# Kernel tuning notes

Measured on AMD Instinct MI355X. Metric: run time of the kernel, lower is better.

## Reference

```python
import jax, jax.numpy as jnp
import numpy as np

N = 1024          # n_nodes
E = 32768         # n_edges (includes N self-loops)
EMBED = 256       # embed_dim
NHEAD = 8
NHID = EMBED // NHEAD  # 32
SLOPE = 0.2       # leaky_relu negative slope
NEG = -1e30       # mask value (finite to keep grads clean)


def setup_inputs() -> dict:
    key = jax.random.key(0)
    k1, k2, k3, k4, k5 = jax.random.split(key, 5)
    h = jax.random.normal(k1, (N, EMBED), dtype=jnp.float32)
    # self-loops first so every destination row has >=1 unmasked edge
    loops = jnp.stack([jnp.arange(N, dtype=jnp.int32)] * 2, axis=1)
    rnd = jax.random.randint(k2, (E - N, 2), 0, N, dtype=jnp.int32)
    edge_index = jnp.concatenate([loops, rnd], axis=0)  # [E, 2] = (r, c)
    W_l = jax.random.normal(k3, (EMBED, NHEAD * NHID), jnp.float32) / np.sqrt(EMBED).astype(np.float32)
    W_r = jax.random.normal(k4, (EMBED, NHEAD * NHID), jnp.float32) / np.sqrt(EMBED).astype(np.float32)
    attn_w = jax.random.normal(k5, (NHID,), jnp.float32) / np.sqrt(NHID).astype(np.float32)
    return {"h": h, "edge_index": edge_index, "W_l": W_l, "W_r": W_r, "attn_w": attn_w}


def reference(h, edge_index, W_l, W_r, attn_w):
    n = h.shape[0]
    g_l = (h @ W_l).reshape(n, NHEAD, NHID)  # [N, H, D]
    g_r = (h @ W_r).reshape(n, NHEAD, NHID)  # [N, H, D]
    # dense all-pairs GATv2 score: g_sum[i, j] = g_l[j] + g_r[i]
    # (matches g_l.repeat(n,1,1) + g_r.repeat_interleave(n, dim=0))
    g_sum = g_l[None, :, :, :] + g_r[:, None, :, :]            # [N, N, H, D]
    e = jnp.einsum('ijhd,d->ijh', jax.nn.leaky_relu(g_sum, SLOPE), attn_w)  # [N, N, H]
    # edge mask: keep only (r, c) pairs present in edge_index
    adj = jnp.zeros((n, n), dtype=bool).at[edge_index[:, 0], edge_index[:, 1]].set(True)
    e = jnp.where(adj[:, :, None], e, NEG)
    a = jax.nn.softmax(e, axis=1)                               # softmax over source nodes j
    # attention-weighted aggregation of source features, concat heads
    out = jnp.einsum('ijh,jhd->ihd', a, g_l).reshape(n, NHEAD * NHID)  # [N, EMBED]
    return out
```

## Files before the change

kernel.cpp:

```cpp
#include <hip/hip_runtime.h>
#include <hip/hip_bf16.h>
#include <stdint.h>

#define NN 1024
#define EMBED 256
#define NHEAD 8
#define NHID 32
#define SLOPE 0.2f

__global__ __launch_bounds__(256) void k_prep(const float* __restrict__ h,
                                              const float* __restrict__ Wl,
                                              const float* __restrict__ Wr,
                                              const int* __restrict__ ei, int E,
                                              float* __restrict__ gl,
                                              float* __restrict__ gr,
                                              unsigned int* __restrict__ adj) {
    const int blk = blockIdx.x;
    const int t = threadIdx.x;

    if (blk < 128) {
        const int z  = blk & 1;
        const int bn = ((blk >> 1) & 3) * 64;
        const int bm = (blk >> 3) * 64;
        const float* W = z ? Wr : Wl;
        float* out = z ? gr : gl;
        const int tx = t & 15;
        const int ty = t >> 4;

        __shared__ float As[16][65];
        __shared__ float Bs[16][65];

        const int ar = t >> 2, ac = (t & 3) << 2;
        const int br = t >> 4, bc = (t & 15) << 2;
        const float* Aptr = &h[(bm + ar) * EMBED + ac];
        const float* Bptr = &W[br * EMBED + bn + bc];

        float acc[4][4];
#pragma unroll
        for (int i = 0; i < 4; ++i)
#pragma unroll
            for (int j = 0; j < 4; ++j) acc[i][j] = 0.f;

        float4 a_reg = *reinterpret_cast<const float4*>(Aptr);
        float4 b_reg = *reinterpret_cast<const float4*>(Bptr);

        for (int k0 = 0; k0 < EMBED; k0 += 16) {
            As[ac + 0][ar] = a_reg.x; As[ac + 1][ar] = a_reg.y;
            As[ac + 2][ar] = a_reg.z; As[ac + 3][ar] = a_reg.w;
            Bs[br][bc + 0] = b_reg.x; Bs[br][bc + 1] = b_reg.y;
            Bs[br][bc + 2] = b_reg.z; Bs[br][bc + 3] = b_reg.w;
            __syncthreads();
            if (k0 + 16 < EMBED) {
                a_reg = *reinterpret_cast<const float4*>(Aptr + k0 + 16);
                b_reg = *reinterpret_cast<const float4*>(Bptr + (size_t)(k0 + 16) * EMBED);
            }
#pragma unroll
            for (int kk = 0; kk < 16; ++kk) {
                float a[4], b[4];
#pragma unroll
                for (int i = 0; i < 4; ++i) a[i] = As[kk][ty * 4 + i];
#pragma unroll
                for (int j = 0; j < 4; ++j) b[j] = Bs[kk][tx * 4 + j];
#pragma unroll
                for (int i = 0; i < 4; ++i)
#pragma unroll
                    for (int j = 0; j < 4; ++j) acc[i][j] += a[i] * b[j];
            }
            __syncthreads();
        }
#pragma unroll
        for (int i = 0; i < 4; ++i) {
            float4 v = make_float4(acc[i][0], acc[i][1], acc[i][2], acc[i][3]);
            *reinterpret_cast<float4*>(&out[(bm + ty * 4 + i) * EMBED + bn + tx * 4]) = v;
        }
    } else {
        const int lo = (blk - 128) * 8;
        __shared__ unsigned int lads[256];
        lads[t] = 0u;
        __syncthreads();

        const int4* ei4 = reinterpret_cast<const int4*>(ei);
        const int nvec = E >> 1;
        int base = 0;
        for (; base + 1024 <= nvec; base += 1024) {
            int4 v0 = ei4[base + t];
            int4 v1 = ei4[base + t + 256];
            int4 v2 = ei4[base + t + 512];
            int4 v3 = ei4[base + t + 768];
#pragma unroll
            for (int u = 0; u < 4; ++u) {
                int4 v = (u == 0) ? v0 : (u == 1) ? v1 : (u == 2) ? v2 : v3;
                int r0 = v.x - lo;
                if ((unsigned)r0 < 8u)
                    atomicOr(&lads[r0 * 32 + ((unsigned)v.y >> 5)], 1u << (v.y & 31));
                int r1 = v.z - lo;
                if ((unsigned)r1 < 8u)
                    atomicOr(&lads[r1 * 32 + ((unsigned)v.w >> 5)], 1u << (v.w & 31));
            }
        }
        for (int idx = base + t; idx < nvec; idx += 256) {
            int4 v = ei4[idx];
            int r0 = v.x - lo;
            if ((unsigned)r0 < 8u)
                atomicOr(&lads[r0 * 32 + ((unsigned)v.y >> 5)], 1u << (v.y & 31));
            int r1 = v.z - lo;
            if ((unsigned)r1 < 8u)
                atomicOr(&lads[r1 * 32 + ((unsigned)v.w >> 5)], 1u << (v.w & 31));
        }
        __syncthreads();
        adj[lo * 32 + t] = lads[t];
    }
}

__global__ __launch_bounds__(256) void k_attn(const float* __restrict__ gl,
                                              const float* __restrict__ gr,
                                              const unsigned int* __restrict__ adj,
                                              const float* __restrict__ attn_w,
                                              float* __restrict__ out) {
    const int i = blockIdx.x;
    const int t = threadIdx.x;

    __shared__ int nbr[NN];
    __shared__ int cnt_s;

    if (t < 64) {
        unsigned int w = (t < 32) ? adj[i * 32 + t] : 0u;
        int c = __popc(w);
        int pre = c;
#pragma unroll
        for (int d = 1; d < 64; d <<= 1) {
            int v = __shfl_up(pre, d);
            if (t >= d) pre += v;
        }
        int off = pre - c;
        if (t == 63) cnt_s = pre;
        while (w) {
            int b = __builtin_ctz(w);
            w &= w - 1;
            nbr[off++] = t * 32 + b;
        }
    }
    __syncthreads();

    const int cnt = cnt_s;
    const float grv = gr[i * EMBED + t];
    const float aw = attn_w[t & 31];

    float m = -3e38f;
    float s = 0.f;
    float acc = 0.f;

    float g[4];
#pragma unroll
    for (int u = 0; u < 4; ++u) {
        int e = u < cnt ? u : 0;
        g[u] = gl[nbr[e] * EMBED + t];
    }

    for (int e0 = 0; e0 < cnt; e0 += 4) {
        float cg[4];
#pragma unroll
        for (int u = 0; u < 4; ++u) cg[u] = g[u];
#pragma unroll
        for (int u = 0; u < 4; ++u) {
            int e = e0 + 4 + u;
            e = e < cnt ? e : 0;
            g[u] = gl[nbr[e] * EMBED + t];
        }
        float p[4];
#pragma unroll
        for (int u = 0; u < 4; ++u) {
            float x = cg[u] + grv;
            float pv = (x > 0.f ? x : SLOPE * x) * aw;
            pv += __shfl_xor(pv, 1);
            pv += __shfl_xor(pv, 2);
            pv += __shfl_xor(pv, 4);
            pv += __shfl_xor(pv, 8);
            pv += __shfl_xor(pv, 16);
            p[u] = pv;
        }
#pragma unroll
        for (int u = 0; u < 4; ++u) {
            if (e0 + u < cnt) {
                float mn = fmaxf(m, p[u]);
                float sc = __expf(m - mn);
                float ev = __expf(p[u] - mn);
                s = s * sc + ev;
                acc = acc * sc + ev * cg[u];
                m = mn;
            }
        }
    }
    out[i * EMBED + t] = acc / s;
}

extern "C" void kernel_launch(void* const* d_in, const int* in_sizes, int n_in,
                              void* d_out, int out_size, void* d_ws, size_t ws_size,
                              hipStream_t stream) {
    const float* h  = (const float*)d_in[0];
    const int*   ei = (const int*)d_in[1];
    const float* Wl = (const float*)d_in[2];
    const float* Wr = (const float*)d_in[3];
    const float* aw = (const float*)d_in[4];
    float* out = (float*)d_out;
    const int E = in_sizes[1] / 2;

    unsigned int* adj = (unsigned int*)d_ws;
    float* gl = (float*)((char*)d_ws + 131072);
    float* gr = gl + NN * EMBED;

    k_prep<<<256, 256, 0, stream>>>(h, Wl, Wr, ei, E, gl, gr, adj);
    k_attn<<<NN, 256, 0, stream>>>(gl, gr, adj, aw, out);
}
```

Baseline: 36.41 us.

## Rebalance prep kernel: smaller GEMM tiles, fewer wider adjacency-build blocks

The GEMM part now uses 32x64 output tiles, so it runs on 256 blocks instead of 128, with each thread computing a 2x4 micro-tile. Only half the threads load the A tile. The adjacency part drops from 128 blocks of 8 rows to 32 blocks of 32 rows, which cuts the redundant full scans of edge_index by a factor of four. The intent is to spread GEMM work across more CUs and shrink total edge-scan traffic. In exchange, each GEMM thread does less reuse per load, and the new scan loop assumes nvec is a multiple of 2048, with the remainder loop removed.

Measured after the change: 38.36 us. 5.3% more time.

```diff
diff --git a/kernel.cpp b/kernel.cpp
--- a/kernel.cpp
+++ b/kernel.cpp
@@ -18,97 +18,90 @@
     const int blk = blockIdx.x;
     const int t = threadIdx.x;
 
-    if (blk < 128) {
+    if (blk < 256) {
         const int z  = blk & 1;
         const int bn = ((blk >> 1) & 3) * 64;
-        const int bm = (blk >> 3) * 64;
+        const int bm = (blk >> 3) * 32;
         const float* W = z ? Wr : Wl;
-        float* out = z ? gr : gl;
+        float* outg = z ? gr : gl;
         const int tx = t & 15;
         const int ty = t >> 4;
 
-        __shared__ float As[16][65];
-        __shared__ float Bs[16][65];
+        __shared__ float As[16][33];
+        __shared__ float Bs[16][68];
+
+        float acc[2][4];
+#pragma unroll
+        for (int i = 0; i < 2; ++i)
+#pragma unroll
+            for (int j = 0; j < 4; ++j) acc[i][j] = 0.f;
 
         const int ar = t >> 2, ac = (t & 3) << 2;
         const int br = t >> 4, bc = (t & 15) << 2;
-        const float* Aptr = &h[(bm + ar) * EMBED + ac];
-        const float* Bptr = &W[br * EMBED + bn + bc];
-
-        float acc[4][4];
-#pragma unroll
-        for (int i = 0; i < 4; ++i)
-#pragma unroll
-            for (int j = 0; j < 4; ++j) acc[i][j] = 0.f;
-
-        float4 a_reg = *reinterpret_cast<const float4*>(Aptr);
-        float4 b_reg = *reinterpret_cast<const float4*>(Bptr);
+        const float* Ap = &h[(bm + ar) * EMBED + ac];
+        const float* Bp = &W[br * EMBED + bn + bc];
+
+        float4 a_reg = make_float4(0.f, 0.f, 0.f, 0.f);
+        if (t < 128) a_reg = *reinterpret_cast<const float4*>(Ap);
+        float4 b_reg = *reinterpret_cast<const float4*>(Bp);
 
         for (int k0 = 0; k0 < EMBED; k0 += 16) {
-            As[ac + 0][ar] = a_reg.x; As[ac + 1][ar] = a_reg.y;
-            As[ac + 2][ar] = a_reg.z; As[ac + 3][ar] = a_reg.w;
+            if (t < 128) {
+                As[ac + 0][ar] = a_reg.x; As[ac + 1][ar] = a_reg.y;
+                As[ac + 2][ar] = a_reg.z; As[ac + 3][ar] = a_reg.w;
+            }
             Bs[br][bc + 0] = b_reg.x; Bs[br][bc + 1] = b_reg.y;
             Bs[br][bc + 2] = b_reg.z; Bs[br][bc + 3] = b_reg.w;
             __syncthreads();
             if (k0 + 16 < EMBED) {
-                a_reg = *reinterpret_cast<const float4*>(Aptr + k0 + 16);
-                b_reg = *reinterpret_cast<const float4*>(Bptr + (size_t)(k0 + 16) * EMBED);
+                if (t < 128) a_reg = *reinterpret_cast<const float4*>(Ap + k0 + 16);
+                b_reg = *reinterpret_cast<const float4*>(Bp + (size_t)(k0 + 16) * EMBED);
             }
 #pragma unroll
             for (int kk = 0; kk < 16; ++kk) {
-                float a[4], b[4];
-#pragma unroll
-                for (int i = 0; i < 4; ++i) a[i] = As[kk][ty * 4 + i];
-#pragma unroll
-                for (int j = 0; j < 4; ++j) b[j] = Bs[kk][tx * 4 + j];
-#pragma unroll
-                for (int i = 0; i < 4; ++i)
-#pragma unroll
-                    for (int j = 0; j < 4; ++j) acc[i][j] += a[i] * b[j];
+                float a0 = As[kk][ty * 2 + 0];
+                float a1 = As[kk][ty * 2 + 1];
+                float b0 = Bs[kk][tx * 4 + 0];
+                float b1 = Bs[kk][tx * 4 + 1];
+                float b2 = Bs[kk][tx * 4 + 2];
+                float b3 = Bs[kk][tx * 4 + 3];
+                acc[0][0] += a0 * b0; acc[0][1] += a0 * b1;
+                acc[0][2] += a0 * b2; acc[0][3] += a0 * b3;
+                acc[1][0] += a1 * b0; acc[1][1] += a1 * b1;
+                acc[1][2] += a1 * b2; acc[1][3] += a1 * b3;
             }
             __syncthreads();
         }
 #pragma unroll
-        for (int i = 0; i < 4; ++i) {
+        for (int i = 0; i < 2; ++i) {
             float4 v = make_float4(acc[i][0], acc[i][1], acc[i][2], acc[i][3]);
-            *reinterpret_cast<float4*>(&out[(bm + ty * 4 + i) * EMBED + bn + tx * 4]) = v;
+            *reinterpret_cast<float4*>(&outg[(bm + ty * 2 + i) * EMBED + bn + tx * 4]) = v;
         }
     } else {
-        const int lo = (blk - 128) * 8;
-        __shared__ unsigned int lads[256];
-        lads[t] = 0u;
+        const int lo = (blk - 256) * 32;
+        __shared__ unsigned int lads[1024];
+#pragma unroll
+        for (int u = 0; u < 4; ++u) lads[t + u * 256] = 0u;
         __syncthreads();
 
         const int4* ei4 = reinterpret_cast<const int4*>(ei);
         const int nvec = E >> 1;
-        int base = 0;
-        for (; base + 1024 <= nvec; base += 1024) {
-            int4 v0 = ei4[base + t];
-            int4 v1 = ei4[base + t + 256];
-            int4 v2 = ei4[base + t + 512];
-            int4 v3 = ei4[base + t + 768];
-#pragma unroll
-            for (int u = 0; u < 4; ++u) {
-                int4 v = (u == 0) ? v0 : (u == 1) ? v1 : (u == 2) ? v2 : v3;
+        for (int base = 0; base < nvec; base += 2048) {
+#pragma unroll 8
+            for (int u = 0; u < 8; ++u) {
+                int4 v = ei4[base + u * 256 + t];
                 int r0 = v.x - lo;
-                if ((unsigned)r0 < 8u)
+                if ((unsigned)r0 < 32u)
                     atomicOr(&lads[r0 * 32 + ((unsigned)v.y >> 5)], 1u << (v.y & 31));
                 int r1 = v.z - lo;
-                if ((unsigned)r1 < 8u)
+                if ((unsigned)r1 < 32u)
                     atomicOr(&lads[r1 * 32 + ((unsigned)v.w >> 5)], 1u << (v.w & 31));
             }
         }
-        for (int idx = base + t; idx < nvec; idx += 256) {
-            int4 v = ei4[idx];
-            int r0 = v.x - lo;
-            if ((unsigned)r0 < 8u)
-                atomicOr(&lads[r0 * 32 + ((unsigned)v.y >> 5)], 1u << (v.y & 31));
-            int r1 = v.z - lo;
-            if ((unsigned)r1 < 8u)
-                atomicOr(&lads[r1 * 32 + ((unsigned)v.w >> 5)], 1u << (v.w & 31));
-        }
         __syncthreads();
-        adj[lo * 32 + t] = lads[t];
+#pragma unroll
+        for (int u = 0; u < 4; ++u)
+            adj[lo * 32 + t + u * 256] = lads[t + u * 256];
     }
 }
 
@@ -209,6 +202,6 @@
     float* gl = (float*)((char*)d_ws + 131072);
     float* gr = gl + NN * EMBED;
 
-    k_prep<<<256, 256, 0, stream>>>(h, Wl, Wr, ei, E, gl, gr, adj);
+    k_prep<<<288, 256, 0, stream>>>(h, Wl, Wr, ei, E, gl, gr, adj);
     k_attn<<<NN, 256, 0, stream>>>(gl, gr, adj, aw, out);
 }
```
